# Kernel optimization log

Measured on AMD Instinct MI355X. Metric: run time of the kernel, lower is better.

## Reference

```python
import jax, jax.numpy as jnp
import numpy as np

REF_MIC_IDX = 0
LOAD = 0.001 / np.sqrt(2.0)  # diagonal loading added to BOTH real and imag parts in the torch code


def setup_inputs() -> dict:
    key = jax.random.key(0)
    k1, k2, k3 = jax.random.split(key, 3)
    shape = (8, 2, 8, 600, 257)  # N, RI, C, T, F
    return {
        "mixture": jax.random.normal(k1, shape, dtype=jnp.float32),
        "target": jax.random.normal(k2, shape, dtype=jnp.float32),
        "noise": jax.random.normal(k3, shape, dtype=jnp.float32),
    }


def _to_complex(x):
    # (N, 2, C, T, F) RI-stacked -> (N, C, T, F) complex
    return jax.lax.complex(x[:, 0], x[:, 1])


def reference(mixture, target, noise):
    N, _, C, T, F = mixture.shape
    y = _to_complex(mixture)  # (N, C, T, F)
    v = _to_complex(noise)
    cdtype = y.dtype

    # Time-averaged spatial covariance: sum_t V V^H / T -> (N, F, C, C)
    # (fused; the original materializes per-frame C x C matrices then sums)
    phi_v = jnp.einsum("nctf,ndtf->nfcd", v, jnp.conj(v)) / T
    phi_y = jnp.einsum("nctf,ndtf->nfcd", y, jnp.conj(y)) / T

    eye = jnp.eye(C, dtype=cdtype)
    # torch adds LOAD*eye to both real and imag slices -> complex (1+1j)*LOAD*eye
    phi_v = phi_v + (LOAD * (1.0 + 1.0j)) * eye

    G = jnp.linalg.inv(phi_v) @ phi_y  # (N, F, C, C)

    # l = trace(G) - C, where torch subtracts scalar C from both RI parts
    l = jnp.trace(G, axis1=-2, axis2=-1) - (C * (1.0 + 1.0j))  # (N, F)

    # H = (1/l) * (G - I) e_ref  -> column ref_mic_idx of (G - I)
    Ge = (G - eye)[..., :, REF_MIC_IDX]  # (N, F, C)
    H = Ge / l[..., None]  # (N, F, C)

    # Beamform: X(n,t,f) = sum_c conj(H)_{n,f,c} * y_{n,c,t,f}
    X = jnp.einsum("nfc,nctf->ntf", jnp.conj(H), y)  # (N, T, F)

    # Output in RI-stacked form with singleton channel: (N, 2, 1, T, F)
    est = jnp.stack([jnp.real(X), jnp.imag(X)], axis=1)[:, :, None]
    return est
```

## Files before the change

kernel.cpp:

```cpp
#include <hip/hip_runtime.h>


constexpr int N_  = 8;
constexpr int C_  = 8;
constexpr int T_  = 600;
constexpr int F_  = 257;
constexpr int TF_  = T_ * F_;
constexpr int CTF_ = C_ * TF_;
constexpr int NSTR_ = 2 * CTF_;
constexpr int NF_  = N_ * F_;
constexpr int NPAIR_ = 36;
constexpr float LOADC_ = 7.0710678118654755e-4f;
constexpr float INV_T_ = 1.0f / 600.0f;

#define SBAR() __builtin_amdgcn_sched_barrier(0)

struct cx { float r, i; };
__device__ __forceinline__ cx cmul(cx a, cx b) { return {a.r*b.r - a.i*b.i, a.r*b.i + a.i*b.r}; }
__device__ __forceinline__ cx csub(cx a, cx b) { return {a.r - b.r, a.i - b.i}; }
__device__ __forceinline__ cx cinv(cx a) {
    float id = 1.0f / (a.r*a.r + a.i*a.i);
    return {a.r*id, -a.i*id};
}
__device__ __forceinline__ cx cmadd(cx acc, cx a, cx b) {
    acc.r += a.r*b.r - a.i*b.i;
    acc.i += a.r*b.i + a.i*b.r;
    return acc;
}

template<int TSPLIT>
__global__ __launch_bounds__(320, 2) void cov_partial(
        const float* __restrict__ mix, const float* __restrict__ noi,
        float* __restrict__ part) {
    constexpr int TCHUNK = T_ / TSPLIT;
    static_assert(TCHUNK % 2 == 0, "TB=2 slabs need even TCHUNK");
    constexpr int NS = TCHUNK / 2;
    constexpr int NE2 = 16 * 257;
    constexpr int KU = 13;

    __shared__ float S[2][16][514];

    const int tid = threadIdx.x;
    const int chunk = blockIdx.x;
    const int n = blockIdx.y;
    const int m = blockIdx.z;
    const float* src = (m ? mix : noi) + (size_t)n * NSTR_;
    const int tBase = chunk * TCHUNK;

    float2 rg[KU];
    auto stage = [&](int t0) {
        const size_t tF = (size_t)t0 * 257;
#pragma unroll
        for (int kk = 0; kk < KU; ++kk) {
            int u = tid + 320 * kk; int e = (u >= NE2) ? u - NE2 : u;
            int pl = e / 257; int r = e - pl * 257;
            int c = pl & 7;
            size_t goff = ((pl < 8) ? (size_t)c * TF_
                                    : (size_t)CTF_ + (size_t)c * TF_) + 2 * r;
            rg[kk] = *(const float2*)(src + goff + tF);
        }
    };
    auto writeL = [&](int buf) {
        float* b = &S[buf][0][0];
#pragma unroll
        for (int kk = 0; kk < KU; ++kk) {
            int u = tid + 320 * kk; int e = (u >= NE2) ? u - NE2 : u;
            int pl = e / 257; int r = e - pl * 257;
            *(float2*)(b + pl * 514 + 2 * r) = rg[kk];
        }
    };

    float accr[NPAIR_], acci[NPAIR_];
#pragma unroll
    for (int p = 0; p < NPAIR_; ++p) { accr[p] = 0.f; acci[p] = 0.f; }

    auto consume = [&](int buf) {
        if (tid < F_) {
#pragma unroll
            for (int tt = 0; tt < 2; ++tt) {
                float re[C_], im[C_];
#pragma unroll
                for (int c = 0; c < C_; ++c) {
                    re[c] = S[buf][c][tt * 257 + tid];
                    im[c] = S[buf][8 + c][tt * 257 + tid];
                }
                int p = 0;
#pragma unroll
                for (int c = 0; c < C_; ++c) {
#pragma unroll
                    for (int d = 0; d <= c; ++d, ++p) {
                        accr[p] += re[c]*re[d] + im[c]*im[d];
                        acci[p] += im[c]*re[d] - re[c]*im[d];
                    }
                }
            }
        }
    };

    stage(tBase); SBAR();
    writeL(0);
    __syncthreads();

    for (int k = 0; k < NS; ++k) {
        const bool more = (k + 1 < NS);
        if (more) { stage(tBase + 2 * (k + 1)); SBAR(); }
        consume(k & 1);
        SBAR();
        if (more) writeL((k + 1) & 1);
        __syncthreads();
    }

    if (tid < F_) {
        float* out = part + (size_t)((m * TSPLIT + chunk) * 72) * NF_ + n * F_ + tid;
#pragma unroll
        for (int p = 0; p < NPAIR_; ++p) {
            out[(size_t)(2*p)   * NF_] = accr[p];
            out[(size_t)(2*p+1) * NF_] = acci[p];
        }
    }
}

__global__ __launch_bounds__(256) void reduce_cov(float* __restrict__ part, int tsplit) {
    int flat = blockIdx.x * 256 + threadIdx.x;
    constexpr int NQ4 = NF_ / 4;
    if (flat >= 2 * 72 * NQ4) return;
    int idx4 = flat % NQ4;
    int z = flat / NQ4;
    int m = z / 72;
    int q = z % 72;
    const float4* p4 = (const float4*)(part) + ((size_t)((m * tsplit) * 72 + q) * NF_) / 4 + idx4;
    float4 s = {0.f, 0.f, 0.f, 0.f};
    for (int ch = 0; ch < tsplit; ++ch) {
        float4 v = p4[(size_t)(ch * 72) * NF_ / 4];
        s.x += v.x; s.y += v.y; s.z += v.z; s.w += v.w;
    }
    *(float4*)((float*)part + (size_t)((m * tsplit) * 72 + q) * NF_ + idx4 * 4) = s;
}

__global__ __launch_bounds__(256) void solve_w(
        const float* __restrict__ part, float* __restrict__ W, size_t yBase) {
    int widx = (blockIdx.x * 256 + threadIdx.x) >> 6;
    if (widx >= NF_) return;
    const int lane = threadIdx.x & 63;
    const int i = lane >> 3, j = lane & 7;

    const float* pv = part + widx;
    const float* py = part + yBase + widx;

    {
        int a = (i > j) ? i : j, b = (i > j) ? j : i;
        int p = a*(a+1)/2 + b;
        float vr = pv[(size_t)(2*p)   * NF_] * INV_T_;
        float vi = pv[(size_t)(2*p+1) * NF_] * INV_T_;
        if (j > i) vi = -vi;
        cx M0 { vr, vi };
        if (i == j) { M0.r += LOADC_; M0.i += LOADC_; }
        cx M = M0;

#pragma unroll
        for (int k = 0; k < 8; ++k) {
            cx mkk { __shfl(M.r, (k<<3)|k, 64), __shfl(M.i, (k<<3)|k, 64) };
            cx mkj { __shfl(M.r, (k<<3)|j, 64), __shfl(M.i, (k<<3)|j, 64) };
            cx mik { __shfl(M.r, (i<<3)|k, 64), __shfl(M.i, (i<<3)|k, 64) };
            cx pk = cinv(mkk);
            cx rk = cmul(mkj, pk);
            if (i == k) {
                M = (j == k) ? pk : rk;
            } else if (j == k) {
                cx t = cmul(mik, pk);
                M = { -t.r, -t.i };
            } else {
                M = csub(M, cmul(mik, rk));
            }
        }

        int ay = (i > j) ? i : j, by = (i > j) ? j : i;
        int pt = ay*(ay+1)/2 + by;
        float yr = py[(size_t)(2*pt)   * NF_] * INV_T_;
        float yi = py[(size_t)(2*pt+1) * NF_] * INV_T_;
        if (i > j) yi = -yi;
        cx Yji { yr, yi };
        cx trt = cmul(M, Yji);
        float tr_r = trt.r, tr_i = trt.i;
#pragma unroll
        for (int off = 1; off < 64; off <<= 1) {
            tr_r += __shfl_xor(tr_r, off, 64);
            tr_i += __shfl_xor(tr_i, off, 64);
        }

        int p0 = j*(j+1)/2;
        cx y0 { py[(size_t)(2*p0)   * NF_] * INV_T_,
                py[(size_t)(2*p0+1) * NF_] * INV_T_ };
        cx g = cmul(M, y0);
#pragma unroll
        for (int off = 1; off < 8; off <<= 1) {
            g.r += __shfl_xor(g.r, off, 64);
            g.i += __shfl_xor(g.i, off, 64);
        }

        cx l { tr_r - 8.0f, tr_i - 8.0f };
        float iden = 1.0f / (l.r*l.r + l.i*l.i);
        if (j == 0) {
            cx ge = g;
            if (i == 0) ge.r -= 1.0f;
            float* w = W + (size_t)widx * 16;
            w[2*i]     = (ge.r*l.r + ge.i*l.i) * iden;
            w[2*i + 1] = (ge.r*l.i - ge.i*l.r) * iden;
        }
    }
}

__global__ __launch_bounds__(256) void beamform(
        const float* __restrict__ mix, const float* __restrict__ W,
        float* __restrict__ out) {
    constexpr int U = TF_ / 4;
    int n = blockIdx.y;
    int u = blockIdx.x * 256 + threadIdx.x;
    if (u >= U) return;
    int j0 = 4 * u;
    int f0 = j0 % F_;

    float4 wv[4][4];
#pragma unroll
    for (int i = 0; i < 4; ++i) {
        int fi = f0 + i; if (fi >= F_) fi -= F_;
        const float4* wr = (const float4*)(W + (size_t)(n * F_ + fi) * 16);
        wv[i][0] = wr[0]; wv[i][1] = wr[1]; wv[i][2] = wr[2]; wv[i][3] = wr[3];
    }

    const float* base = mix + (size_t)n * NSTR_ + j0;
    float xr[4] = {0.f,0.f,0.f,0.f}, xi[4] = {0.f,0.f,0.f,0.f};
#pragma unroll
    for (int c = 0; c < C_; ++c) {
        float4 yr4 = *(const float4*)(base + (size_t)c * TF_);
        float4 yi4 = *(const float4*)(base + (size_t)c * TF_ + CTF_);
        float yrA[4] = {yr4.x, yr4.y, yr4.z, yr4.w};
        float yiA[4] = {yi4.x, yi4.y, yi4.z, yi4.w};
#pragma unroll
        for (int i = 0; i < 4; ++i) {
            float wr_ = (c & 1) ? wv[i][c >> 1].z : wv[i][c >> 1].x;
            float wi_ = (c & 1) ? wv[i][c >> 1].w : wv[i][c >> 1].y;
            xr[i] += wr_*yrA[i] - wi_*yiA[i];
            xi[i] += wr_*yiA[i] + wi_*yrA[i];
        }
    }
    float* op = out + (size_t)n * (2 * TF_);
    *(float4*)(op + j0)       = make_float4(xr[0], xr[1], xr[2], xr[3]);
    *(float4*)(op + TF_ + j0) = make_float4(xi[0], xi[1], xi[2], xi[3]);
}

extern "C" void kernel_launch(void* const* d_in, const int* in_sizes, int n_in,
                              void* d_out, int out_size, void* d_ws, size_t ws_size,
                              hipStream_t stream) {
    const float* mix = (const float*)d_in[0];
    const float* noi = (const float*)d_in[2];

    const size_t need30 = ((size_t)2 * 30 * 72 * NF_ + (size_t)16 * NF_) * 4;
    float* part = (float*)d_ws;
    int tsplit;
    if (ws_size >= need30) {
        tsplit = 30;
        cov_partial<30><<<dim3(30, N_, 2), 320, 0, stream>>>(mix, noi, part);
    } else {
        tsplit = 25;
        cov_partial<25><<<dim3(25, N_, 2), 320, 0, stream>>>(mix, noi, part);
    }
    float* W = part + (size_t)2 * tsplit * 72 * NF_;

    reduce_cov<<<dim3((2 * 72 * (NF_ / 4) + 255) / 256), 256, 0, stream>>>(part, tsplit);
    solve_w<<<dim3((NF_ * 64 + 255) / 256), 256, 0, stream>>>(part, W, (size_t)tsplit * 72 * NF_);
    beamform<<<dim3((TF_ / 4 + 255) / 256, N_), 256, 0, stream>>>(mix, W, (float*)d_out);
}
```

Before: 252.2 us.

## Widen covariance slabs to four frames, batch reduce and beamform loads

The covariance kernel now stages four time frames per slab with float4 global loads and a larger LDS buffer. This halves the number of sync iterations and widens memory transactions, and launch bounds drop to one block per SIMD to fit the bigger shared buffer. The reduce kernel issues up to ten partial loads before summing, and the beamformer hoists all 16 mixture loads ahead of the weight loads to raise memory-level parallelism. The cost is higher LDS and register use, which lowers occupancy.

```diff
diff --git a/kernel.cpp b/kernel.cpp
--- a/kernel.cpp
+++ b/kernel.cpp
@@ -22,23 +22,18 @@
     float id = 1.0f / (a.r*a.r + a.i*a.i);
     return {a.r*id, -a.i*id};
 }
-__device__ __forceinline__ cx cmadd(cx acc, cx a, cx b) {
-    acc.r += a.r*b.r - a.i*b.i;
-    acc.i += a.r*b.i + a.i*b.r;
-    return acc;
-}
 
 template<int TSPLIT>
-__global__ __launch_bounds__(320, 2) void cov_partial(
+__global__ __launch_bounds__(320, 1) void cov_partial(
         const float* __restrict__ mix, const float* __restrict__ noi,
         float* __restrict__ part) {
     constexpr int TCHUNK = T_ / TSPLIT;
-    static_assert(TCHUNK % 2 == 0, "TB=2 slabs need even TCHUNK");
-    constexpr int NS = TCHUNK / 2;
-    constexpr int NE2 = 16 * 257;
+    static_assert(TCHUNK % 4 == 0, "4t slabs need TCHUNK % 4 == 0");
+    constexpr int NS = TCHUNK / 4;
+    constexpr int NE4 = 16 * 257;
     constexpr int KU = 13;
 
-    __shared__ float S[2][16][514];
+    __shared__ float S[2][16][1028];
 
     const int tid = threadIdx.x;
     const int chunk = blockIdx.x;
@@ -47,26 +42,26 @@
     const float* src = (m ? mix : noi) + (size_t)n * NSTR_;
     const int tBase = chunk * TCHUNK;
 
-    float2 rg[KU];
+    float4 rg[KU];
     auto stage = [&](int t0) {
         const size_t tF = (size_t)t0 * 257;
 #pragma unroll
         for (int kk = 0; kk < KU; ++kk) {
-            int u = tid + 320 * kk; int e = (u >= NE2) ? u - NE2 : u;
+            int u = tid + 320 * kk; int e = (u >= NE4) ? u - NE4 : u;
             int pl = e / 257; int r = e - pl * 257;
             int c = pl & 7;
             size_t goff = ((pl < 8) ? (size_t)c * TF_
-                                    : (size_t)CTF_ + (size_t)c * TF_) + 2 * r;
-            rg[kk] = *(const float2*)(src + goff + tF);
+                                    : (size_t)CTF_ + (size_t)c * TF_) + 4 * r;
+            rg[kk] = *(const float4*)(src + goff + tF);
         }
     };
     auto writeL = [&](int buf) {
         float* b = &S[buf][0][0];
 #pragma unroll
         for (int kk = 0; kk < KU; ++kk) {
-            int u = tid + 320 * kk; int e = (u >= NE2) ? u - NE2 : u;
+            int u = tid + 320 * kk; int e = (u >= NE4) ? u - NE4 : u;
             int pl = e / 257; int r = e - pl * 257;
-            *(float2*)(b + pl * 514 + 2 * r) = rg[kk];
+            *(float4*)(b + pl * 1028 + 4 * r) = rg[kk];
         }
     };
 
@@ -77,7 +72,7 @@
     auto consume = [&](int buf) {
         if (tid < F_) {
 #pragma unroll
-            for (int tt = 0; tt < 2; ++tt) {
+            for (int tt = 0; tt < 4; ++tt) {
                 float re[C_], im[C_];
 #pragma unroll
                 for (int c = 0; c < C_; ++c) {
@@ -103,7 +98,7 @@
 
     for (int k = 0; k < NS; ++k) {
         const bool more = (k + 1 < NS);
-        if (more) { stage(tBase + 2 * (k + 1)); SBAR(); }
+        if (more) { stage(tBase + 4 * (k + 1)); SBAR(); }
         consume(k & 1);
         SBAR();
         if (more) writeL((k + 1) & 1);
@@ -130,9 +125,16 @@
     int q = z % 72;
     const float4* p4 = (const float4*)(part) + ((size_t)((m * tsplit) * 72 + q) * NF_) / 4 + idx4;
     float4 s = {0.f, 0.f, 0.f, 0.f};
-    for (int ch = 0; ch < tsplit; ++ch) {
-        float4 v = p4[(size_t)(ch * 72) * NF_ / 4];
-        s.x += v.x; s.y += v.y; s.z += v.z; s.w += v.w;
+    for (int ch0 = 0; ch0 < tsplit; ch0 += 10) {
+        int nb = tsplit - ch0; if (nb > 10) nb = 10;
+        float4 v[10];
+#pragma unroll
+        for (int k = 0; k < 10; ++k)
+            if (k < nb) v[k] = p4[(size_t)((ch0 + k) * 72) * NF_ / 4];
+        SBAR();
+#pragma unroll
+        for (int k = 0; k < 10; ++k)
+            if (k < nb) { s.x += v[k].x; s.y += v[k].y; s.z += v[k].z; s.w += v[k].w; }
     }
     *(float4*)((float*)part + (size_t)((m * tsplit) * 72 + q) * NF_ + idx4 * 4) = s;
 }
@@ -147,66 +149,62 @@
     const float* pv = part + widx;
     const float* py = part + yBase + widx;
 
-    {
-        int a = (i > j) ? i : j, b = (i > j) ? j : i;
-        int p = a*(a+1)/2 + b;
-        float vr = pv[(size_t)(2*p)   * NF_] * INV_T_;
-        float vi = pv[(size_t)(2*p+1) * NF_] * INV_T_;
-        if (j > i) vi = -vi;
-        cx M0 { vr, vi };
-        if (i == j) { M0.r += LOADC_; M0.i += LOADC_; }
-        cx M = M0;
-
-#pragma unroll
-        for (int k = 0; k < 8; ++k) {
-            cx mkk { __shfl(M.r, (k<<3)|k, 64), __shfl(M.i, (k<<3)|k, 64) };
-            cx mkj { __shfl(M.r, (k<<3)|j, 64), __shfl(M.i, (k<<3)|j, 64) };
-            cx mik { __shfl(M.r, (i<<3)|k, 64), __shfl(M.i, (i<<3)|k, 64) };
-            cx pk = cinv(mkk);
-            cx rk = cmul(mkj, pk);
-            if (i == k) {
-                M = (j == k) ? pk : rk;
-            } else if (j == k) {
-                cx t = cmul(mik, pk);
-                M = { -t.r, -t.i };
-            } else {
-                M = csub(M, cmul(mik, rk));
-            }
-        }
-
-        int ay = (i > j) ? i : j, by = (i > j) ? j : i;
-        int pt = ay*(ay+1)/2 + by;
-        float yr = py[(size_t)(2*pt)   * NF_] * INV_T_;
-        float yi = py[(size_t)(2*pt+1) * NF_] * INV_T_;
-        if (i > j) yi = -yi;
-        cx Yji { yr, yi };
-        cx trt = cmul(M, Yji);
-        float tr_r = trt.r, tr_i = trt.i;
-#pragma unroll
-        for (int off = 1; off < 64; off <<= 1) {
-            tr_r += __shfl_xor(tr_r, off, 64);
-            tr_i += __shfl_xor(tr_i, off, 64);
-        }
-
-        int p0 = j*(j+1)/2;
-        cx y0 { py[(size_t)(2*p0)   * NF_] * INV_T_,
-                py[(size_t)(2*p0+1) * NF_] * INV_T_ };
-        cx g = cmul(M, y0);
-#pragma unroll
-        for (int off = 1; off < 8; off <<= 1) {
-            g.r += __shfl_xor(g.r, off, 64);
-            g.i += __shfl_xor(g.i, off, 64);
-        }
-
-        cx l { tr_r - 8.0f, tr_i - 8.0f };
-        float iden = 1.0f / (l.r*l.r + l.i*l.i);
-        if (j == 0) {
-            cx ge = g;
-            if (i == 0) ge.r -= 1.0f;
-            float* w = W + (size_t)widx * 16;
-            w[2*i]     = (ge.r*l.r + ge.i*l.i) * iden;
-            w[2*i + 1] = (ge.r*l.i - ge.i*l.r) * iden;
-        }
+    int a = (i > j) ? i : j, b = (i > j) ? j : i;
+    int p = a*(a+1)/2 + b;
+    float vr = pv[(size_t)(2*p)   * NF_] * INV_T_;
+    float vi = pv[(size_t)(2*p+1) * NF_] * INV_T_;
+    if (j > i) vi = -vi;
+    cx M { vr, vi };
+    if (i == j) { M.r += LOADC_; M.i += LOADC_; }
+
+#pragma unroll
+    for (int k = 0; k < 8; ++k) {
+        cx mkk { __shfl(M.r, (k<<3)|k, 64), __shfl(M.i, (k<<3)|k, 64) };
+        cx mkj { __shfl(M.r, (k<<3)|j, 64), __shfl(M.i, (k<<3)|j, 64) };
+        cx mik { __shfl(M.r, (i<<3)|k, 64), __shfl(M.i, (i<<3)|k, 64) };
+        cx pk = cinv(mkk);
+        cx rk = cmul(mkj, pk);
+        if (i == k) {
+            M = (j == k) ? pk : rk;
+        } else if (j == k) {
+            cx t = cmul(mik, pk);
+            M = { -t.r, -t.i };
+        } else {
+            M = csub(M, cmul(mik, rk));
+        }
+    }
+
+    int pt = a*(a+1)/2 + b;
+    float yr = py[(size_t)(2*pt)   * NF_] * INV_T_;
+    float yi = py[(size_t)(2*pt+1) * NF_] * INV_T_;
+    if (i > j) yi = -yi;
+    cx Yji { yr, yi };
+    cx trt = cmul(M, Yji);
+    float tr_r = trt.r, tr_i = trt.i;
+#pragma unroll
+    for (int off = 1; off < 64; off <<= 1) {
+        tr_r += __shfl_xor(tr_r, off, 64);
+        tr_i += __shfl_xor(tr_i, off, 64);
+    }
+
+    int p0 = j*(j+1)/2;
+    cx y0 { py[(size_t)(2*p0)   * NF_] * INV_T_,
+            py[(size_t)(2*p0+1) * NF_] * INV_T_ };
+    cx g = cmul(M, y0);
+#pragma unroll
+    for (int off = 1; off < 8; off <<= 1) {
+        g.r += __shfl_xor(g.r, off, 64);
+        g.i += __shfl_xor(g.i, off, 64);
+    }
+
+    cx l { tr_r - 8.0f, tr_i - 8.0f };
+    float iden = 1.0f / (l.r*l.r + l.i*l.i);
+    if (j == 0) {
+        cx ge = g;
+        if (i == 0) ge.r -= 1.0f;
+        float* w = W + (size_t)widx * 16;
+        w[2*i]     = (ge.r*l.r + ge.i*l.i) * iden;
+        w[2*i + 1] = (ge.r*l.i - ge.i*l.r) * iden;
     }
 }
 
@@ -220,6 +218,15 @@
     int j0 = 4 * u;
     int f0 = j0 % F_;
 
+    const float* base = mix + (size_t)n * NSTR_ + j0;
+    float4 y[16];
+#pragma unroll
+    for (int c = 0; c < C_; ++c) {
+        y[c]     = *(const float4*)(base + (size_t)c * TF_);
+        y[8 + c] = *(const float4*)(base + (size_t)c * TF_ + CTF_);
+    }
+    SBAR();
+
     float4 wv[4][4];
 #pragma unroll
     for (int i = 0; i < 4; ++i) {
@@ -228,14 +235,11 @@
         wv[i][0] = wr[0]; wv[i][1] = wr[1]; wv[i][2] = wr[2]; wv[i][3] = wr[3];
     }
 
-    const float* base = mix + (size_t)n * NSTR_ + j0;
     float xr[4] = {0.f,0.f,0.f,0.f}, xi[4] = {0.f,0.f,0.f,0.f};
 #pragma unroll
     for (int c = 0; c < C_; ++c) {
-        float4 yr4 = *(const float4*)(base + (size_t)c * TF_);
-        float4 yi4 = *(const float4*)(base + (size_t)c * TF_ + CTF_);
-        float yrA[4] = {yr4.x, yr4.y, yr4.z, yr4.w};
-        float yiA[4] = {yi4.x, yi4.y, yi4.z, yi4.w};
+        float yrA[4] = {y[c].x, y[c].y, y[c].z, y[c].w};
+        float yiA[4] = {y[8+c].x, y[8+c].y, y[8+c].z, y[8+c].w};
 #pragma unroll
         for (int i = 0; i < 4; ++i) {
             float wr_ = (c & 1) ? wv[i][c >> 1].z : wv[i][c >> 1].x;
```

Result: slower. 286.4 us (+13.6%).
